# Kernel tuning notes

Hardware: AMD Instinct MI355X
Metric: run time of the kernel (lower is better)

Reference implementation:

```python
import jax, jax.numpy as jnp
import numpy as np

K = 9
HF = WF = 128
SAMPLING = 16
H_IMG = W_IMG = 2048.0
ANC_RATIO = np.array([0.5, 1.0, 2.0])
ANC_SIZE = np.array([8.0, 16.0, 32.0])
TOPN_NMS = 6000
N_NMS = 2000
THR_NMS = 0.7


def generate_anchors():
    # loop order in original GenerateAnchor: ii over Wf (ctrx), jj over Hf (ctry), ratio, size
    ctrx = (np.arange(WF) + 0.5) * SAMPLING  # [Wf]
    ctry = (np.arange(HF) + 0.5) * SAMPLING  # [Hf]
    w = SAMPLING * ANC_SIZE[None, :] / np.sqrt(ANC_RATIO)[:, None]  # [R,S]
    h = SAMPLING * ANC_SIZE[None, :] * np.sqrt(ANC_RATIO)[:, None]
    cx = ctrx[:, None, None, None]  # [Wf,1,1,1]
    cy = ctry[None, :, None, None]  # [1,Hf,1,1]
    w = w[None, None]; h = h[None, None]  # [1,1,R,S]
    x1, y1 = cx - w / 2, cy - h / 2
    x2, y2 = cx + w / 2, cy + h / 2
    anc = np.stack(np.broadcast_arrays(x1, y1, x2, y2), axis=-1).reshape(-1, 4)
    return np.round(anc).astype(np.float32)  # [Wf*Hf*K, 4]


def conv2d(x, w, b, pad):
    y = jax.lax.conv_general_dilated(
        x, w, (1, 1), [(pad, pad), (pad, pad)],
        dimension_numbers=('NCHW', 'OIHW', 'NCHW'))
    return y + b[None, :, None, None]


def pairwise_iou(b):
    # Faithful to my_IoU: 'gt' (pivot, row i) coords are int-truncated;
    # intersection via min(all)+w_a+w_g-max(all); union uses raw/truncated areas.
    ax1, ay1, ax2, ay2 = b[:, 0], b[:, 1], b[:, 2], b[:, 3]
    aw, ah = ax2 - ax1, ay2 - ay1
    aminx, amaxx = jnp.minimum(ax1, ax2), jnp.maximum(ax1, ax2)
    aminy, amaxy = jnp.minimum(ay1, ay2), jnp.maximum(ay1, ay2)
    tx1, ty1, tx2, ty2 = jnp.trunc(ax1), jnp.trunc(ay1), jnp.trunc(ax2), jnp.trunc(ay2)
    gminx, gmaxx = jnp.minimum(tx1, tx2), jnp.maximum(tx1, tx2)
    gminy, gmaxy = jnp.minimum(ty1, ty2), jnp.maximum(ty1, ty2)
    gw, gh = jnp.trunc(ax2 - ax1), jnp.trunc(ay2 - ay1)
    iw = jnp.maximum(jnp.minimum(aminx[None, :], gminx[:, None]) + aw[None, :]
                     + gw[:, None] - jnp.maximum(amaxx[None, :], gmaxx[:, None]), 0.0)
    ih = jnp.maximum(jnp.minimum(aminy[None, :], gminy[:, None]) + ah[None, :]
                     + gh[:, None] - jnp.maximum(amaxy[None, :], gmaxy[:, None]), 0.0)
    inter = iw * ih  # [i=pivot, j=candidate]
    union = (aw * ah)[None, :] + (gw * gh)[:, None] - inter
    return inter / union


def make_roi(anchor, delta, obj):
    # delta2xy
    aw = anchor[:, 2] - anchor[:, 0]
    ah = anchor[:, 3] - anchor[:, 1]
    acx = anchor[:, 0] + aw / 2
    acy = anchor[:, 1] + ah / 2
    cx = delta[:, 0] * aw + acx
    cy = delta[:, 1] * ah + acy
    w = jnp.exp(delta[:, 2]) * aw
    h = jnp.exp(delta[:, 3]) * ah
    roi = jnp.stack([cx - w / 2, cy - h / 2, cx + w / 2, cy + h / 2], axis=1)
    # clip exactly as original: negatives->0; >H -> H-1; >W -> W-1
    roi = jnp.maximum(roi, 0.0)
    roi = roi.at[:, 3].set(jnp.where(roi[:, 3] > H_IMG, H_IMG - 1.0, roi[:, 3]))
    roi = roi.at[:, 2].set(jnp.where(roi[:, 2] > W_IMG, W_IMG - 1.0, roi[:, 2]))
    valid = (roi[:, 2] - roi[:, 0] > SAMPLING) & (roi[:, 3] - roi[:, 1] > SAMPLING)
    scores = jnp.where(valid, obj, -jnp.inf)  # mask instead of dropping (jit-friendly)
    top_scores, top_idx = jax.lax.top_k(scores, TOPN_NMS)
    boxes = roi[top_idx]
    keep0 = jnp.isfinite(top_scores)
    iou = pairwise_iou(boxes)  # [TOPN, TOPN]
    idxs = jnp.arange(TOPN_NMS)

    def body(i, keep):
        sup = keep[i] & (iou[i] >= THR_NMS) & (idxs > i)
        return keep & ~sup

    keep = jax.lax.fori_loop(0, TOPN_NMS, body, keep0)
    rank = jnp.cumsum(keep) - 1
    pos = jnp.where(keep & (rank < N_NMS), rank, N_NMS)  # out-of-range rows dropped
    out = jnp.zeros((N_NMS, 4), boxes.dtype).at[pos].set(boxes, mode='drop')
    return out


def setup_inputs() -> dict:
    key = jax.random.key(0)
    ks = jax.random.split(key, 4)
    featmap = jax.random.normal(ks[0], (1, 512, HF, WF), dtype=jnp.float32)
    conv3_w = jax.random.normal(ks[1], (512, 512, 3, 3), dtype=jnp.float32) * 0.01
    conv3_b = jnp.zeros((512,), jnp.float32)
    cls_w = jax.random.normal(ks[2], (2 * K, 512, 1, 1), dtype=jnp.float32) * 0.01
    cls_b = jnp.zeros((2 * K,), jnp.float32)
    reg_w = jax.random.normal(ks[3], (4 * K, 512, 1, 1), dtype=jnp.float32) * 0.01
    reg_b = jnp.zeros((4 * K,), jnp.float32)
    return {'featmap': featmap, 'conv3_w': conv3_w, 'conv3_b': conv3_b,
            'cls_w': cls_w, 'cls_b': cls_b, 'reg_w': reg_w, 'reg_b': reg_b}


def reference(featmap, conv3_w, conv3_b, cls_w, cls_b, reg_w, reg_b):
    x = jax.nn.relu(conv2d(featmap, conv3_w, conv3_b, 1))
    pred_cls = conv2d(x, cls_w, cls_b, 0)  # [1, 2k, Hf, Wf]
    pred_reg = conv2d(x, reg_w, reg_b, 0)  # [1, 4k, Hf, Wf]
    pred_cls = jnp.transpose(pred_cls, (0, 2, 3, 1)).reshape(1, -1, 2)
    pred_reg = jnp.transpose(pred_reg, (0, 2, 3, 1)).reshape(1, -1, 4)
    pred_obj = pred_cls[:, :, 1]
    anchors = jnp.asarray(generate_anchors())
    # roi path is detached in the original (uses .data)
    roi = make_roi(anchors,
                   jax.lax.stop_gradient(pred_reg[0]),
                   jax.lax.stop_gradient(pred_obj[0]))
    return roi, pred_cls, pred_reg
```

## Files before the change

### kernel.cpp

```cpp
#include <hip/hip_runtime.h>

#define HF 128
#define WF 128
#define KANC 9
#define NANC (HF*WF*KANC)
#define NSORT 262144
#define TOPN 6000
#define NWORDS 94
#define NOUT 2000
#define OFF_CLS 8000
#define OFF_REG 302912
#define NCAND 8192
#define NBCAP 2048

typedef unsigned long long u64;
typedef double d4 __attribute__((ext_vector_type(4)));
typedef const __attribute__((address_space(1))) void* gas1;
typedef __attribute__((address_space(3))) void* las3;

__global__ __launch_bounds__(256) void zinit_k(double* p1, int n1,
                                               unsigned* hist, u64* selp,
                                               unsigned* cnt) {
  int i = blockIdx.x * 256 + threadIdx.x;
  if (i < n1) p1[i] = 0.0;
  if (i < 2048) hist[i] = 0;
  if (i == 0) { selp[0] = 0; selp[1] = 0; cnt[0] = 0; cnt[1] = 0; }
}

__global__ __launch_bounds__(256) void wtrans_k(const float* __restrict__ w,
                                                float* __restrict__ wt) {
  __shared__ float ld[64 * 73];
  int t = threadIdx.x;
  int ocg = blockIdx.x & 7, icg = blockIdx.x >> 3;
  int oc0 = ocg << 6, ic0 = icg << 3;
  #pragma unroll
  for (int rep = 0; rep < 18; ++rep) {
    int idx = rep * 256 + t;
    int row = idx / 72, col = idx - row * 72;
    ld[row * 73 + col] = w[(size_t)(oc0 + row) * 4608 + ic0 * 9 + col];
  }
  __syncthreads();
  #pragma unroll
  for (int rep = 0; rep < 18; ++rep) {
    int idx = rep * 256 + t;
    int pair = idx >> 6, oc = idx & 63;
    int tap = pair % 9, ic = pair / 9;
    wt[(size_t)tap * 262144 + (size_t)(ic0 + ic) * 512 + oc0 + oc] =
        ld[oc * 73 + ic * 9 + tap];
  }
}

#define BKC 32
#define NCHUNK 144

__global__ __launch_bounds__(256, 4) void conv_mfma_k(
    const float* __restrict__ feat, const float* __restrict__ wt,
    const float* __restrict__ conv_b, const float* __restrict__ cls_w,
    const float* __restrict__ reg_w, double* __restrict__ predacc)
{
  __shared__ __align__(16) char smraw[32768];
  float* AsB = (float*)smraw;
  float* BsB = (float*)(smraw + 2 * 2048 * 4);
  int tid = threadIdx.x;
  int bid = blockIdx.x;
  int pt = bid & 255, ot = bid >> 8;
  int h = pt >> 1, w0 = (pt & 1) << 6;
  int oc0 = ot << 6;
  int wv = tid >> 6, l = tid & 63;
  int wr = wv >> 1, wc = wv & 1;
  int lg = l >> 4, lr = l & 15;

  d4 acc[2][2];
  #pragma unroll
  for (int t = 0; t < 2; ++t)
    #pragma unroll
    for (int u = 0; u < 2; ++u) acc[t][u] = (d4)0.0;

  float4 areg[2];

  auto gloadA = [&](int c) {
    int tap = c >> 4, ic0 = (c & 15) << 5;
    int kh = tap / 3 - 1, kw = tap % 3 - 1;
    int hp = h + kh;
    bool okh = ((unsigned)hp < 128u);
    #pragma unroll
    for (int i = 0; i < 2; ++i) {
      int q = tid + (i << 8);
      int r = q >> 4, c0 = (q & 15) << 2;
      float v0 = 0.f, v1 = 0.f, v2 = 0.f, v3 = 0.f;
      const float* src = &feat[((ic0 + r) << 14) + (hp << 7)];
      int wp = w0 + c0 + kw;
      if (okh) {
        if ((unsigned)(wp + 0) < 128u) v0 = src[wp + 0];
        if ((unsigned)(wp + 1) < 128u) v1 = src[wp + 1];
        if ((unsigned)(wp + 2) < 128u) v2 = src[wp + 2];
        if ((unsigned)(wp + 3) < 128u) v3 = src[wp + 3];
      }
      areg[i] = make_float4(v0, v1, v2, v3);
    }
  };
  auto gloadB_lds = [&](int c, int buf) {
    float* B = BsB + buf * 2048;
    #pragma unroll
    for (int i = 0; i < 2; ++i) {
      int q = tid + (i << 8);
      int r = q >> 4, c0 = (q & 15) << 2;
      const float* src =
          &wt[(size_t)((c << 5) + r) * 512 + oc0 + (c0 ^ ((r & 1) << 4))];
      __builtin_amdgcn_global_load_lds((gas1)src, (las3)&B[q << 2], 16, 0, 0);
    }
  };
  auto dswriteA = [&](int buf) {
    float* A = AsB + buf * 2048;
    #pragma unroll
    for (int i = 0; i < 2; ++i) {
      int q = tid + (i << 8);
      int r = q >> 4, c0 = (q & 15) << 2;
      *(float4*)&A[(r << 6) + (c0 ^ ((r & 1) << 4))] = areg[i];
    }
  };
  auto compute = [&](int buf) {
    const float* A = AsB + buf * 2048;
    const float* B = BsB + buf * 2048;
    #pragma unroll
    for (int k4 = 0; k4 < BKC; k4 += 4) {
      int krow = k4 + lg;
      int sw = (krow & 1) << 4;
      double a0 = (double)A[(krow << 6) + (((wr << 5) + lr) ^ sw)];
      double a1 = (double)A[(krow << 6) + (((wr << 5) + 16 + lr) ^ sw)];
      double b0 = (double)B[(krow << 6) + (((wc << 5) + lr) ^ sw)];
      double b1 = (double)B[(krow << 6) + (((wc << 5) + 16 + lr) ^ sw)];
      acc[0][0] = __builtin_amdgcn_mfma_f64_16x16x4f64(a0, b0, acc[0][0], 0, 0, 0);
      acc[0][1] = __builtin_amdgcn_mfma_f64_16x16x4f64(a0, b1, acc[0][1], 0, 0, 0);
      acc[1][0] = __builtin_amdgcn_mfma_f64_16x16x4f64(a1, b0, acc[1][0], 0, 0, 0);
      acc[1][1] = __builtin_amdgcn_mfma_f64_16x16x4f64(a1, b1, acc[1][1], 0, 0, 0);
    }
  };

  gloadA(0);
  gloadB_lds(0, 0);
  dswriteA(0);
  for (int c = 0; c < NCHUNK; ++c) {
    __syncthreads();
    if (c + 1 < NCHUNK) {
      gloadB_lds(c + 1, (c + 1) & 1);
      gloadA(c + 1);
    }
    compute(c & 1);
    if (c + 1 < NCHUNK) dswriteA((c + 1) & 1);
  }

  int rmap[4], cmap[4];
  {
    d4 z = (d4)0.0;
    double apr = (lg == 0) ? (double)lr : 0.0;
    double bpr = (lg == 0) ? 1.0 : 0.0;
    d4 dr = __builtin_amdgcn_mfma_f64_16x16x4f64(apr, bpr, z, 0, 0, 0);
    double apc = (lg == 0) ? 1.0 : 0.0;
    double bpc = (lg == 0) ? (double)lr : 0.0;
    d4 dc = __builtin_amdgcn_mfma_f64_16x16x4f64(apc, bpc, z, 0, 0, 0);
    #pragma unroll
    for (int r = 0; r < 4; ++r) { rmap[r] = (int)dr[r]; cmap[r] = (int)dc[r]; }
  }

  double* xs = (double*)smraw;
  float* hwS = (float*)(smraw + 32 * 65 * 8);
  __syncthreads();
  for (int e = tid; e < 54 * 64; e += 256) {
    int o = e >> 6, j = e & 63;
    hwS[e] = (o < 18) ? cls_w[(o << 9) + oc0 + j]
                      : reg_w[((o - 18) << 9) + oc0 + j];
  }
  int pixbase = (h << 7) + w0;
  #pragma unroll
  for (int ph = 0; ph < 2; ++ph) {
    if (wr == ph) {
      #pragma unroll
      for (int t = 0; t < 2; ++t) {
        #pragma unroll
        for (int u = 0; u < 2; ++u) {
          #pragma unroll
          for (int r = 0; r < 4; ++r) {
            int ocl = (wc << 5) + (u << 4) + cmap[r];
            int pxl = (t << 4) + rmap[r];
            double v = acc[t][u][r] + (double)conv_b[oc0 + ocl];
            xs[pxl * 65 + ocl] = (v > 0.0) ? v : 0.0;
          }
        }
      }
    }
    __syncthreads();
    #pragma unroll
    for (int it = 0; it < 7; ++it) {
      int e = tid + (it << 8);
      if (e < 54 * 32) {
        int o = e >> 5, px = e & 31;
        const double* xr = &xs[px * 65];
        const float* hr = &hwS[o << 6];
        double s = 0.0;
        #pragma unroll
        for (int j = 0; j < 64; ++j) s += xr[j] * (double)hr[j];
        atomicAdd(&predacc[(size_t)(pixbase + (ph << 5) + px) * 54 + o], s);
      }
    }
    __syncthreads();
  }
}

__global__ __launch_bounds__(256) void anchor_k(
    const double* __restrict__ predacc, const float* __restrict__ cls_b,
    const float* __restrict__ reg_b, float* __restrict__ out,
    double* __restrict__ roi_all, double* __restrict__ scores_d,
    ulonglong2* __restrict__ sortb)
{
  #pragma clang fp contract(off)
  int a = blockIdx.x * 256 + threadIdx.x;
  if (a >= NSORT) return;
  if (a >= NANC) {
    sortb[a] = make_ulonglong2(0xFFF0000000000000ULL, 0xFFFFFFFFULL);
    return;
  }
  int pix = a / 9;
  int k = a - pix * 9;
  int h = pix >> 7, wq = pix & 127;
  const double* pa = &predacc[pix * 54];
  double c0 = pa[2 * k] + (double)cls_b[2 * k];
  double c1 = pa[2 * k + 1] + (double)cls_b[2 * k + 1];
  double d0 = pa[18 + 4 * k + 0] + (double)reg_b[4 * k + 0];
  double d1 = pa[18 + 4 * k + 1] + (double)reg_b[4 * k + 1];
  double d2 = pa[18 + 4 * k + 2] + (double)reg_b[4 * k + 2];
  double d3 = pa[18 + 4 * k + 3] + (double)reg_b[4 * k + 3];
  out[OFF_CLS + a * 2 + 0] = (float)c0;
  out[OFF_CLS + a * 2 + 1] = (float)c1;
  out[OFF_REG + a * 4 + 0] = (float)d0;
  out[OFF_REG + a * 4 + 1] = (float)d1;
  out[OFF_REG + a * 4 + 2] = (float)d2;
  out[OFF_REG + a * 4 + 3] = (float)d3;
  int ir = k / 3, is = k - ir * 3;
  double ratio = (ir == 0) ? 0.5 : (ir == 1 ? 1.0 : 2.0);
  double asz = (is == 0) ? 8.0 : (is == 1 ? 16.0 : 32.0);
  double sq = sqrt(ratio);
  double wa = (16.0 * asz) / sq;
  double ha = (16.0 * asz) * sq;
  double cx = (h + 0.5) * 16.0;
  double cy = (wq + 0.5) * 16.0;
  double A0 = (double)(float)rint(cx - wa * 0.5);
  double A1 = (double)(float)rint(cy - ha * 0.5);
  double A2 = (double)(float)rint(cx + wa * 0.5);
  double A3 = (double)(float)rint(cy + ha * 0.5);
  double aw = A2 - A0, ah = A3 - A1;
  double acx = A0 + aw * 0.5, acy = A1 + ah * 0.5;
  double ccx = d0 * aw + acx;
  double ccy = d1 * ah + acy;
  double wr = exp(d2) * aw;
  double hh = exp(d3) * ah;
  double r0 = ccx - wr * 0.5;
  double r1 = ccy - hh * 0.5;
  double r2 = ccx + wr * 0.5;
  double r3 = ccy + hh * 0.5;
  r0 = fmax(r0, 0.0); r1 = fmax(r1, 0.0); r2 = fmax(r2, 0.0); r3 = fmax(r3, 0.0);
  r3 = (r3 > 2048.0) ? 2047.0 : r3;
  r2 = (r2 > 2048.0) ? 2047.0 : r2;
  bool valid = ((r2 - r0) > 16.0) && ((r3 - r1) > 16.0);
  double score = valid ? c1 : -__builtin_huge_val();
  roi_all[a * 4 + 0] = r0;
  roi_all[a * 4 + 1] = r1;
  roi_all[a * 4 + 2] = r2;
  roi_all[a * 4 + 3] = r3;
  scores_d[a] = score;
  u64 u = (u64)__double_as_longlong(score);
  u64 m = (u >> 63) ? ~u : (u | 0x8000000000000000ULL);
  sortb[a] = make_ulonglong2(~m, (u64)a);
}

__global__ __launch_bounds__(1024) void hist_k(const ulonglong2* __restrict__ sortb,
                                               unsigned* __restrict__ hist,
                                               const u64* __restrict__ selp,
                                               int pass) {
  __shared__ unsigned h[2048];
  int t = threadIdx.x;
  h[t] = 0; h[t + 1024] = 0;
  __syncthreads();
  const int SH[3] = {53, 42, 31};
  const u64 PM[3] = {0ULL, 0xFFE0000000000000ULL, 0xFFFFFC0000000000ULL};
  u64 pfx = selp[0];
  u64 pm = PM[pass];
  int sh = SH[pass];
  for (int e = blockIdx.x * 1024 + t; e < NSORT; e += gridDim.x * 1024) {
    u64 k = sortb[e].x;
    if ((k & pm) == pfx)
      atomicAdd(&h[(unsigned)((k >> sh) & 2047)], 1u);
  }
  __syncthreads();
  if (h[t]) atomicAdd(&hist[t], h[t]);
  if (h[t + 1024]) atomicAdd(&hist[t + 1024], h[t + 1024]);
}

__global__ __launch_bounds__(1024) void scan_k(unsigned* hist, u64* selp, int pass) {
  __shared__ unsigned h[2048];
  int t = threadIdx.x;
  h[t] = hist[t]; h[t + 1024] = hist[t + 1024];
  hist[t] = 0; hist[t + 1024] = 0;
  __syncthreads();
  if (t == 0) {
    const int SH[3] = {53, 42, 31};
    u64 cum = selp[1];
    u64 pfx = selp[0];
    int b = 0;
    for (; b < 2047; ++b) {
      if (cum + h[b] >= (u64)TOPN) break;
      cum += h[b];
    }
    selp[0] = pfx | ((u64)b << SH[pass]);
    selp[1] = cum;
  }
}

__global__ __launch_bounds__(1024) void compact_k(
    const ulonglong2* __restrict__ sortb, const u64* __restrict__ selp,
    ulonglong2* __restrict__ cand, ulonglong2* __restrict__ bcand,
    unsigned* __restrict__ cnt) {
  u64 pfx = selp[0];
  const u64 M33 = 0xFFFFFFFF80000000ULL;
  for (int e = blockIdx.x * 1024 + threadIdx.x; e < NSORT; e += gridDim.x * 1024) {
    ulonglong2 v = sortb[e];
    u64 top = v.x & M33;
    if (top < pfx) {
      unsigned p = atomicAdd(&cnt[0], 1u);
      if (p < NCAND) cand[p] = v;
    } else if (top == pfx) {
      unsigned p = atomicAdd(&cnt[1], 1u);
      if (p < NBCAP) bcand[p] = v;
    }
  }
}

__device__ __forceinline__ bool sless(ulonglong2 A, ulonglong2 B) {
  return (A.x < B.x) || (A.x == B.x && A.y < B.y);
}

__global__ __launch_bounds__(1024) void sortloc_k(
    ulonglong2* cand, const ulonglong2* __restrict__ bcand,
    const unsigned* __restrict__ cnt) {
  __shared__ ulonglong2 s[2048];
  int t = threadIdx.x;
  int base = blockIdx.x * 2048;
  unsigned ci = cnt[0]; if (ci > NCAND) ci = NCAND;
  unsigned cb = cnt[1]; if (cb > NBCAP) cb = NBCAP;
  #pragma unroll
  for (int i = 0; i < 2; ++i) {
    int p = base + t + (i << 10);
    ulonglong2 v;
    if (p < (int)ci) v = cand[p];
    else if (p < (int)(ci + cb)) v = bcand[p - ci];
    else v = make_ulonglong2(~0ULL, ~0ULL);
    s[t + (i << 10)] = v;
  }
  __syncthreads();
  for (int k = 2; k <= 2048; k <<= 1)
    for (int j = k >> 1; j >= 1; j >>= 1) {
      int li = ((t & ~(j - 1)) << 1) | (t & (j - 1));
      int pa = li | j;
      bool asc = (((base + li) & k) == 0);
      ulonglong2 A = s[li], B = s[pa];
      bool sw = asc ? sless(B, A) : sless(A, B);
      if (sw) { s[li] = B; s[pa] = A; }
      __syncthreads();
    }
  cand[base + t] = s[t];
  cand[base + t + 1024] = s[t + 1024];
}

__global__ __launch_bounds__(256) void bitonic_global(ulonglong2* d, int k, int j) {
  int t = blockIdx.x * 256 + threadIdx.x;
  int i = ((t & ~(j - 1)) << 1) | (t & (j - 1));
  int p = i | j;
  bool asc = ((i & k) == 0);
  ulonglong2 A = d[i], B = d[p];
  bool sw = asc ? sless(B, A) : sless(A, B);
  if (sw) { d[i] = B; d[p] = A; }
}

__global__ __launch_bounds__(1024) void bitonic_lm(ulonglong2* d, int k) {
  __shared__ ulonglong2 s[2048];
  int t = threadIdx.x;
  int base = blockIdx.x * 2048;
  bool asc = ((base & k) == 0);
  s[t] = d[base + t];
  s[t + 1024] = d[base + t + 1024];
  __syncthreads();
  for (int j = 1024; j >= 1; j >>= 1) {
    int li = ((t & ~(j - 1)) << 1) | (t & (j - 1));
    int pa = li | j;
    ulonglong2 A = s[li], B = s[pa];
    bool sw = asc ? sless(B, A) : sless(A, B);
    if (sw) { s[li] = B; s[pa] = A; }
    __syncthreads();
  }
  d[base + t] = s[t];
  d[base + t + 1024] = s[t + 1024];
}

__global__ __launch_bounds__(1024) void sortfin_k(
    ulonglong2* d, const double* __restrict__ roi_all,
    const double* __restrict__ scores_d, double* __restrict__ boxes,
    u64* __restrict__ removed) {
  __shared__ ulonglong2 s[2048];
  int t = threadIdx.x;
  int base = blockIdx.x * 2048;
  s[t] = d[base + t];
  s[t + 1024] = d[base + t + 1024];
  __syncthreads();
  for (int j = 1024; j >= 1; j >>= 1) {
    int li = ((t & ~(j - 1)) << 1) | (t & (j - 1));
    int pa = li | j;
    ulonglong2 A = s[li], B = s[pa];
    if (sless(B, A)) { s[li] = B; s[pa] = A; }
    __syncthreads();
  }
  #pragma unroll
  for (int q = 0; q < 2; ++q) {
    int li = t + (q << 10);
    int i = base + li;
    if (i < TOPN) {
      unsigned idx = (unsigned)s[li].y;
      double b0 = 0, b1 = 0, b2 = 0, b3 = 0;
      if (idx < NANC) {
        b0 = roi_all[idx * 4 + 0];
        b1 = roi_all[idx * 4 + 1];
        b2 = roi_all[idx * 4 + 2];
        b3 = roi_all[idx * 4 + 3];
      }
      boxes[i * 4 + 0] = b0; boxes[i * 4 + 1] = b1;
      boxes[i * 4 + 2] = b2; boxes[i * 4 + 3] = b3;
    }
  }
  if (t < 32) {
    int w = (base >> 6) + t;
    if (w < NWORDS) {
      u64 wdd = (w == NWORDS - 1) ? 0xFFFF000000000000ULL : 0ULL;
      for (int b = 0; b < 64; ++b) {
        int i = w * 64 + b;
        if (i >= TOPN) break;
        unsigned idx = (unsigned)s[i - base].y;
        bool dead = true;
        if (idx < NANC) dead = isinf(scores_d[idx]);
        if (dead) wdd |= (1ULL << b);
      }
      removed[w] = wdd;
    }
  }
}

__global__ __launch_bounds__(256) void mask_k(const double* __restrict__ boxes,
                                              u64* __restrict__ mask) {
  #pragma clang fp contract(off)
  int gw = (blockIdx.x * 256 + threadIdx.x) >> 6;
  int lane = threadIdx.x & 63;
  int i = gw / NWORDS, wj = gw - i * NWORDS;
  if (i >= TOPN) return;
  if (wj < (i >> 6)) return;
  double ix1 = boxes[i * 4 + 0], iy1 = boxes[i * 4 + 1];
  double ix2 = boxes[i * 4 + 2], iy2 = boxes[i * 4 + 3];
  double tx1 = trunc(ix1), ty1 = trunc(iy1), tx2 = trunc(ix2), ty2 = trunc(iy2);
  double gminx = fmin(tx1, tx2), gmaxx = fmax(tx1, tx2);
  double gminy = fmin(ty1, ty2), gmaxy = fmax(ty1, ty2);
  double gw_ = trunc(ix2 - ix1), gh_ = trunc(iy2 - iy1);
  int j = wj * 64 + lane;
  bool pred = false;
  if (j < TOPN && j > i) {
    double jx1 = boxes[j * 4 + 0], jy1 = boxes[j * 4 + 1];
    double jx2 = boxes[j * 4 + 2], jy2 = boxes[j * 4 + 3];
    double aw = jx2 - jx1, ah = jy2 - jy1;
    double aminx = fmin(jx1, jx2), amaxx = fmax(jx1, jx2);
    double aminy = fmin(jy1, jy2), amaxy = fmax(jy1, jy2);
    double iw = fmin(aminx, gminx) + aw + gw_ - fmax(amaxx, gmaxx);
    iw = fmax(iw, 0.0);
    double ih = fmin(aminy, gminy) + ah + gh_ - fmax(amaxy, gmaxy);
    ih = fmax(ih, 0.0);
    double inter = iw * ih;
    double uni = aw * ah + gw_ * gh_ - inter;
    pred = (inter / uni >= 0.7);
  }
  u64 bal = __ballot(pred);
  if (lane == 0) mask[(size_t)i * NWORDS + wj] = bal;
}

__global__ __launch_bounds__(1024) void nmsout_k(const u64* __restrict__ mask,
                                                 const u64* __restrict__ removed_g,
                                                 const double* __restrict__ boxes,
                                                 float* __restrict__ out) {
  __shared__ u64 rem[NWORDS];
  __shared__ u64 aliveSh;
  __shared__ int pref[NWORDS + 1];
  int t = threadIdx.x;
  int lane = t & 63;
  int wvid = t >> 6;
  if (t < NWORDS) rem[t] = removed_g[t];
  for (int i = t; i < NOUT * 4; i += 1024) out[i] = 0.0f;
  __syncthreads();
  for (int c = 0; c < NWORDS; ++c) {
    if (wvid == 0) {
      int i = c * 64 + lane;
      u64 diag = (i < TOPN) ? mask[(size_t)i * NWORDS + c] : 0ULL;
      u64 local = rem[c];
      #pragma unroll 1
      for (int j = 0; j < 64; ++j) {
        u64 dj = __shfl(diag, j);
        if (!((local >> j) & 1ULL)) local |= dj;
      }
      if (lane == 0) { rem[c] = local; aliveSh = ~local; }
    }
    __syncthreads();
    u64 alive = aliveSh;
    int nw = NWORDS - 1 - c;
    if (nw > 0 && alive) {
      int npairs = 64 * nw;
      for (int p = t; p < npairs; p += 1024) {
        int j = p / nw;
        int w = c + 1 + (p - j * nw);
        if ((alive >> j) & 1ULL) {
          int i = c * 64 + j;
          if (i < TOPN) {
            u64 v = mask[(size_t)i * NWORDS + w];
            if (v) atomicOr(&rem[w], v);
          }
        }
      }
    }
    __syncthreads();
  }
  if (t == 0) {
    int s = 0;
    for (int w = 0; w < NWORDS; ++w) { pref[w] = s; s += __popcll(~rem[w]); }
    pref[NWORDS] = s;
  }
  __syncthreads();
  for (int i = t; i < TOPN; i += 1024) {
    u64 kw = ~rem[i >> 6];
    if ((kw >> (i & 63)) & 1ULL) {
      int rank = pref[i >> 6] + __popcll(kw & ((1ULL << (i & 63)) - 1ULL));
      if (rank < NOUT) {
        out[rank * 4 + 0] = (float)boxes[i * 4 + 0];
        out[rank * 4 + 1] = (float)boxes[i * 4 + 1];
        out[rank * 4 + 2] = (float)boxes[i * 4 + 2];
        out[rank * 4 + 3] = (float)boxes[i * 4 + 3];
      }
    }
  }
}

extern "C" void kernel_launch(void* const* d_in, const int* in_sizes, int n_in,
                              void* d_out, int out_size, void* d_ws, size_t ws_size,
                              hipStream_t stream) {
  const float* feat = (const float*)d_in[0];
  const float* c3w = (const float*)d_in[1];
  const float* c3b = (const float*)d_in[2];
  const float* clw = (const float*)d_in[3];
  const float* clb = (const float*)d_in[4];
  const float* rgw = (const float*)d_in[5];
  const float* rgb = (const float*)d_in[6];
  float* out = (float*)d_out;
  char* ws = (char*)d_ws;
  size_t off = 0;
  auto alloc = [&](size_t bytes) {
    size_t o = off;
    off = (off + bytes + 255) & ~(size_t)255;
    return o;
  };
  double* predacc = (double*)(ws + alloc(16384ULL * 54 * 8));
  float* wt = (float*)(ws + alloc(2359296ULL * 4));
  double* roi_all = (double*)(ws + alloc((size_t)NANC * 4 * 8));
  double* scores_d = (double*)(ws + alloc((size_t)NANC * 8));
  ulonglong2* sortb = (ulonglong2*)(ws + alloc((size_t)NSORT * 16));
  double* boxes = (double*)(ws + alloc((size_t)TOPN * 4 * 8));
  u64* mask = (u64*)(ws + alloc((size_t)TOPN * NWORDS * 8));
  u64* removed = (u64*)(ws + alloc(NWORDS * 8));
  unsigned* hist = (unsigned*)(ws + alloc(2048 * 4));
  u64* selp = (u64*)(ws + alloc(256));
  unsigned* cntb = (unsigned*)(ws + alloc(256));
  ulonglong2* cand = (ulonglong2*)(ws + alloc((size_t)NCAND * 16));
  ulonglong2* bcand = (ulonglong2*)(ws + alloc((size_t)NBCAP * 16));
  (void)ws_size; (void)out_size; (void)in_sizes; (void)n_in;

  const int NPRED = 16384 * 54;
  hipLaunchKernelGGL(zinit_k, dim3((NPRED + 255) / 256), dim3(256), 0, stream,
                     predacc, NPRED, hist, selp, cntb);
  hipLaunchKernelGGL(wtrans_k, dim3(512), dim3(256), 0, stream, c3w, wt);
  hipLaunchKernelGGL(conv_mfma_k, dim3(2048), dim3(256), 0, stream,
                     feat, wt, c3b, clw, rgw, predacc);
  hipLaunchKernelGGL(anchor_k, dim3(NSORT / 256), dim3(256), 0, stream,
                     predacc, clb, rgb, out, roi_all, scores_d, sortb);
  for (int pass = 0; pass < 3; ++pass) {
    hipLaunchKernelGGL(hist_k, dim3(128), dim3(1024), 0, stream,
                       sortb, hist, selp, pass);
    hipLaunchKernelGGL(scan_k, dim3(1), dim3(1024), 0, stream, hist, selp, pass);
  }
  hipLaunchKernelGGL(compact_k, dim3(128), dim3(1024), 0, stream,
                     sortb, selp, cand, bcand, cntb);
  hipLaunchKernelGGL(sortloc_k, dim3(4), dim3(1024), 0, stream,
                     cand, bcand, cntb);
  hipLaunchKernelGGL(bitonic_global, dim3(NCAND / 512), dim3(256), 0, stream,
                     cand, 4096, 2048);
  hipLaunchKernelGGL(bitonic_lm, dim3(4), dim3(1024), 0, stream, cand, 4096);
  hipLaunchKernelGGL(bitonic_global, dim3(NCAND / 512), dim3(256), 0, stream,
                     cand, 8192, 4096);
  hipLaunchKernelGGL(bitonic_global, dim3(NCAND / 512), dim3(256), 0, stream,
                     cand, 8192, 2048);
  hipLaunchKernelGGL(sortfin_k, dim3(4), dim3(1024), 0, stream,
                     cand, roi_all, scores_d, boxes, removed);
  hipLaunchKernelGGL(mask_k, dim3(TOPN * NWORDS / 4), dim3(256), 0, stream,
                     boxes, mask);
  hipLaunchKernelGGL(nmsout_k, dim3(1), dim3(1024), 0, stream,
                     mask, removed, boxes, out);
}
```

Before: 2.267 ms.

## Fuse first radix histogram into anchor kernel, raise MFMA priority, enlarge mask blocks

The anchor kernel now builds the first-pass 11-bit key histogram in shared memory and merges it into the global histogram with atomics, which removes one hist_k launch and one re-read of the sort buffer. The conv compute loop is wrapped in s_setprio to favour MFMA-issuing waves over waves doing loads. mask_k moves from 256-thread to 1024-thread blocks to cut the block count. All three changes are small compared with the conv kernel, which dominates total time. The fused histogram adds LDS atomics and a global atomic flush per block.

```diff
diff --git a/kernel.cpp b/kernel.cpp
--- a/kernel.cpp
+++ b/kernel.cpp
@@ -122,6 +122,7 @@
   auto compute = [&](int buf) {
     const float* A = AsB + buf * 2048;
     const float* B = BsB + buf * 2048;
+    __builtin_amdgcn_s_setprio(1);
     #pragma unroll
     for (int k4 = 0; k4 < BKC; k4 += 4) {
       int krow = k4 + lg;
@@ -135,6 +136,7 @@
       acc[1][0] = __builtin_amdgcn_mfma_f64_16x16x4f64(a1, b0, acc[1][0], 0, 0, 0);
       acc[1][1] = __builtin_amdgcn_mfma_f64_16x16x4f64(a1, b1, acc[1][1], 0, 0, 0);
     }
+    __builtin_amdgcn_s_setprio(0);
   };
 
   gloadA(0);
@@ -211,66 +213,81 @@
     const double* __restrict__ predacc, const float* __restrict__ cls_b,
     const float* __restrict__ reg_b, float* __restrict__ out,
     double* __restrict__ roi_all, double* __restrict__ scores_d,
-    ulonglong2* __restrict__ sortb)
+    ulonglong2* __restrict__ sortb, unsigned* __restrict__ hist)
 {
   #pragma clang fp contract(off)
-  int a = blockIdx.x * 256 + threadIdx.x;
-  if (a >= NSORT) return;
+  __shared__ unsigned hloc[2048];
+  int tid = threadIdx.x;
+  #pragma unroll
+  for (int i = 0; i < 8; ++i) hloc[tid + (i << 8)] = 0;
+  __syncthreads();
+
+  int a = blockIdx.x * 256 + tid;
+  u64 key;
   if (a >= NANC) {
-    sortb[a] = make_ulonglong2(0xFFF0000000000000ULL, 0xFFFFFFFFULL);
-    return;
-  }
-  int pix = a / 9;
-  int k = a - pix * 9;
-  int h = pix >> 7, wq = pix & 127;
-  const double* pa = &predacc[pix * 54];
-  double c0 = pa[2 * k] + (double)cls_b[2 * k];
-  double c1 = pa[2 * k + 1] + (double)cls_b[2 * k + 1];
-  double d0 = pa[18 + 4 * k + 0] + (double)reg_b[4 * k + 0];
-  double d1 = pa[18 + 4 * k + 1] + (double)reg_b[4 * k + 1];
-  double d2 = pa[18 + 4 * k + 2] + (double)reg_b[4 * k + 2];
-  double d3 = pa[18 + 4 * k + 3] + (double)reg_b[4 * k + 3];
-  out[OFF_CLS + a * 2 + 0] = (float)c0;
-  out[OFF_CLS + a * 2 + 1] = (float)c1;
-  out[OFF_REG + a * 4 + 0] = (float)d0;
-  out[OFF_REG + a * 4 + 1] = (float)d1;
-  out[OFF_REG + a * 4 + 2] = (float)d2;
-  out[OFF_REG + a * 4 + 3] = (float)d3;
-  int ir = k / 3, is = k - ir * 3;
-  double ratio = (ir == 0) ? 0.5 : (ir == 1 ? 1.0 : 2.0);
-  double asz = (is == 0) ? 8.0 : (is == 1 ? 16.0 : 32.0);
-  double sq = sqrt(ratio);
-  double wa = (16.0 * asz) / sq;
-  double ha = (16.0 * asz) * sq;
-  double cx = (h + 0.5) * 16.0;
-  double cy = (wq + 0.5) * 16.0;
-  double A0 = (double)(float)rint(cx - wa * 0.5);
-  double A1 = (double)(float)rint(cy - ha * 0.5);
-  double A2 = (double)(float)rint(cx + wa * 0.5);
-  double A3 = (double)(float)rint(cy + ha * 0.5);
-  double aw = A2 - A0, ah = A3 - A1;
-  double acx = A0 + aw * 0.5, acy = A1 + ah * 0.5;
-  double ccx = d0 * aw + acx;
-  double ccy = d1 * ah + acy;
-  double wr = exp(d2) * aw;
-  double hh = exp(d3) * ah;
-  double r0 = ccx - wr * 0.5;
-  double r1 = ccy - hh * 0.5;
-  double r2 = ccx + wr * 0.5;
-  double r3 = ccy + hh * 0.5;
-  r0 = fmax(r0, 0.0); r1 = fmax(r1, 0.0); r2 = fmax(r2, 0.0); r3 = fmax(r3, 0.0);
-  r3 = (r3 > 2048.0) ? 2047.0 : r3;
-  r2 = (r2 > 2048.0) ? 2047.0 : r2;
-  bool valid = ((r2 - r0) > 16.0) && ((r3 - r1) > 16.0);
-  double score = valid ? c1 : -__builtin_huge_val();
-  roi_all[a * 4 + 0] = r0;
-  roi_all[a * 4 + 1] = r1;
-  roi_all[a * 4 + 2] = r2;
-  roi_all[a * 4 + 3] = r3;
-  scores_d[a] = score;
-  u64 u = (u64)__double_as_longlong(score);
-  u64 m = (u >> 63) ? ~u : (u | 0x8000000000000000ULL);
-  sortb[a] = make_ulonglong2(~m, (u64)a);
+    key = 0xFFF0000000000000ULL;
+    if (a < NSORT) sortb[a] = make_ulonglong2(key, 0xFFFFFFFFULL);
+  } else {
+    int pix = a / 9;
+    int k = a - pix * 9;
+    int h = pix >> 7, wq = pix & 127;
+    const double* pa = &predacc[pix * 54];
+    double c0 = pa[2 * k] + (double)cls_b[2 * k];
+    double c1 = pa[2 * k + 1] + (double)cls_b[2 * k + 1];
+    double d0 = pa[18 + 4 * k + 0] + (double)reg_b[4 * k + 0];
+    double d1 = pa[18 + 4 * k + 1] + (double)reg_b[4 * k + 1];
+    double d2 = pa[18 + 4 * k + 2] + (double)reg_b[4 * k + 2];
+    double d3 = pa[18 + 4 * k + 3] + (double)reg_b[4 * k + 3];
+    out[OFF_CLS + a * 2 + 0] = (float)c0;
+    out[OFF_CLS + a * 2 + 1] = (float)c1;
+    out[OFF_REG + a * 4 + 0] = (float)d0;
+    out[OFF_REG + a * 4 + 1] = (float)d1;
+    out[OFF_REG + a * 4 + 2] = (float)d2;
+    out[OFF_REG + a * 4 + 3] = (float)d3;
+    int ir = k / 3, is = k - ir * 3;
+    double ratio = (ir == 0) ? 0.5 : (ir == 1 ? 1.0 : 2.0);
+    double asz = (is == 0) ? 8.0 : (is == 1 ? 16.0 : 32.0);
+    double sq = sqrt(ratio);
+    double wa = (16.0 * asz) / sq;
+    double ha = (16.0 * asz) * sq;
+    double cx = (h + 0.5) * 16.0;
+    double cy = (wq + 0.5) * 16.0;
+    double A0 = (double)(float)rint(cx - wa * 0.5);
+    double A1 = (double)(float)rint(cy - ha * 0.5);
+    double A2 = (double)(float)rint(cx + wa * 0.5);
+    double A3 = (double)(float)rint(cy + ha * 0.5);
+    double aw = A2 - A0, ah = A3 - A1;
+    double acx = A0 + aw * 0.5, acy = A1 + ah * 0.5;
+    double ccx = d0 * aw + acx;
+    double ccy = d1 * ah + acy;
+    double wr = exp(d2) * aw;
+    double hh = exp(d3) * ah;
+    double r0 = ccx - wr * 0.5;
+    double r1 = ccy - hh * 0.5;
+    double r2 = ccx + wr * 0.5;
+    double r3 = ccy + hh * 0.5;
+    r0 = fmax(r0, 0.0); r1 = fmax(r1, 0.0); r2 = fmax(r2, 0.0); r3 = fmax(r3, 0.0);
+    r3 = (r3 > 2048.0) ? 2047.0 : r3;
+    r2 = (r2 > 2048.0) ? 2047.0 : r2;
+    bool valid = ((r2 - r0) > 16.0) && ((r3 - r1) > 16.0);
+    double score = valid ? c1 : -__builtin_huge_val();
+    roi_all[a * 4 + 0] = r0;
+    roi_all[a * 4 + 1] = r1;
+    roi_all[a * 4 + 2] = r2;
+    roi_all[a * 4 + 3] = r3;
+    scores_d[a] = score;
+    u64 u = (u64)__double_as_longlong(score);
+    u64 m = (u >> 63) ? ~u : (u | 0x8000000000000000ULL);
+    key = ~m;
+    sortb[a] = make_ulonglong2(key, (u64)a);
+  }
+  atomicAdd(&hloc[(unsigned)((key >> 53) & 2047)], 1u);
+  __syncthreads();
+  #pragma unroll
+  for (int i = 0; i < 8; ++i) {
+    int b = tid + (i << 8);
+    if (hloc[b]) atomicAdd(&hist[b], hloc[b]);
+  }
 }
 
 __global__ __launch_bounds__(1024) void hist_k(const ulonglong2* __restrict__ sortb,
@@ -452,10 +469,10 @@
   }
 }
 
-__global__ __launch_bounds__(256) void mask_k(const double* __restrict__ boxes,
-                                              u64* __restrict__ mask) {
+__global__ __launch_bounds__(1024) void mask_k(const double* __restrict__ boxes,
+                                               u64* __restrict__ mask) {
   #pragma clang fp contract(off)
-  int gw = (blockIdx.x * 256 + threadIdx.x) >> 6;
+  int gw = (blockIdx.x * 1024 + threadIdx.x) >> 6;
   int lane = threadIdx.x & 63;
   int i = gw / NWORDS, wj = gw - i * NWORDS;
   if (i >= TOPN) return;
@@ -590,8 +607,9 @@
   hipLaunchKernelGGL(conv_mfma_k, dim3(2048), dim3(256), 0, stream,
                      feat, wt, c3b, clw, rgw, predacc);
   hipLaunchKernelGGL(anchor_k, dim3(NSORT / 256), dim3(256), 0, stream,
-                     predacc, clb, rgb, out, roi_all, scores_d, sortb);
-  for (int pass = 0; pass < 3; ++pass) {
+                     predacc, clb, rgb, out, roi_all, scores_d, sortb, hist);
+  hipLaunchKernelGGL(scan_k, dim3(1), dim3(1024), 0, stream, hist, selp, 0);
+  for (int pass = 1; pass < 3; ++pass) {
     hipLaunchKernelGGL(hist_k, dim3(128), dim3(1024), 0, stream,
                        sortb, hist, selp, pass);
     hipLaunchKernelGGL(scan_k, dim3(1), dim3(1024), 0, stream, hist, selp, pass);
@@ -609,7 +627,7 @@
                      cand, 8192, 2048);
   hipLaunchKernelGGL(sortfin_k, dim3(4), dim3(1024), 0, stream,
                      cand, roi_all, scores_d, boxes, removed);
-  hipLaunchKernelGGL(mask_k, dim3(TOPN * NWORDS / 4), dim3(256), 0, stream,
+  hipLaunchKernelGGL(mask_k, dim3(TOPN * NWORDS / 16), dim3(1024), 0, stream,
                      boxes, mask);
   hipLaunchKernelGGL(nmsout_k, dim3(1), dim3(1024), 0, stream,
                      mask, removed, boxes, out);
```

Result: slower. 2.331 ms (+2.8%).
